# Optimization experiments

Hardware: AMD Instinct MI355X
Metric: run time of the kernel (lower is better)

## Reference

```python
import jax, jax.numpy as jnp
import numpy as np

B, C, N, K = 4, 256, 8192, 16
H, S = 8, 2            # num_heads, num_scale
HC = C // H            # head_channels = 32
CS = C // S            # per-scale channels = 128
HS = H // S            # heads per scale = 4
KV_CH = (64, 128)
EPS = 1e-5
SCALE = HC ** -0.5


def setup_inputs() -> dict:
    key = jax.random.key(0)
    ks = jax.random.split(key, 20)
    d = {}
    d["x"] = jax.random.normal(ks[0], (B, C, N), jnp.float32)
    d["y0"] = jax.random.normal(ks[1], (B, KV_CH[0], N, K), jnp.float32)
    d["y1"] = jax.random.normal(ks[2], (B, KV_CH[1], N, K), jnp.float32)
    d["q_w"] = jax.random.normal(ks[3], (C, C), jnp.float32) * 0.02
    for i, c in enumerate(KV_CH):
        kk = jax.random.split(ks[4 + i], 4)
        d[f"conv{i}_w"] = jax.random.normal(kk[0], (CS, c), jnp.float32) * 0.05  # 1x1 conv
        d[f"bn{i}_g"] = jnp.ones((CS,), jnp.float32)
        d[f"bn{i}_b"] = jnp.zeros((CS,), jnp.float32)
        d[f"bn{i}_m"] = jax.random.normal(kk[1], (CS,), jnp.float32) * 0.1
        d[f"bn{i}_v"] = jax.random.uniform(kk[2], (CS,), jnp.float32) + 0.5
        d[f"kv{i}_w"] = jax.random.normal(kk[3], (2 * CS, CS), jnp.float32) * 0.02
    d["proj_w"] = jax.random.normal(ks[8], (C, C), jnp.float32) * 0.02
    d["proj_b"] = jnp.zeros((C,), jnp.float32)
    return d


def _scale_branch(q_i, y, conv_w, g, b, m, v, kv_w):
    # q_i: [B, HS, N, HC];  y: [B, c, N, K]
    z = jnp.einsum('bcnk,oc->bonk', y, conv_w)                 # 1x1 conv -> [B, CS, N, K]
    inv = (g / jnp.sqrt(v + EPS))[None, :, None, None]
    z = jax.nn.relu((z - m[None, :, None, None]) * inv + b[None, :, None, None])
    kv = jnp.transpose(z, (0, 2, 3, 1)) @ kv_w.T               # [B, N, K, 2*CS]
    kv = kv.reshape(B, N, K, HS, HC, 2)
    k = jnp.transpose(kv[..., 0], (0, 3, 1, 2, 4))             # [B, HS, N, K, HC]
    vv = jnp.transpose(kv[..., 1], (0, 3, 1, 2, 4))            # [B, HS, N, K, HC]
    attn = jax.nn.softmax(jnp.einsum('bhnd,bhnkd->bhnk', q_i, k) * SCALE, axis=-1)
    out = jnp.einsum('bhnk,bhnkd->bhnd', attn, vv)             # [B, HS, N, HC]
    return jnp.transpose(out, (0, 2, 1, 3)).reshape(B, N, HS * HC)


def reference(x, y0, y1, q_w,
              conv0_w, bn0_g, bn0_b, bn0_m, bn0_v, kv0_w,
              conv1_w, bn1_g, bn1_b, bn1_m, bn1_v, kv1_w,
              proj_w, proj_b):
    xt = jnp.swapaxes(x, 1, 2)                                 # [B, N, C]
    q = (xt @ q_w.T).reshape(B, N, H, HC).transpose(0, 2, 1, 3)  # [B, H, N, HC]
    o0 = _scale_branch(q[:, :HS], y0, conv0_w, bn0_g, bn0_b, bn0_m, bn0_v, kv0_w)
    o1 = _scale_branch(q[:, HS:], y1, conv1_w, bn1_g, bn1_b, bn1_m, bn1_v, kv1_w)
    outs = jnp.concatenate([o0, o1], axis=-1)                  # [B, N, C]
    outs = outs @ proj_w.T + proj_b
    return jnp.swapaxes(outs, 1, 2)                            # [B, C, N]
```

## Files before the change

### kernel.cpp

```cpp
#include <hip/hip_runtime.h>
#include <hip/hip_bf16.h>

typedef __attribute__((ext_vector_type(8))) short bf16x8;
typedef __attribute__((ext_vector_type(4))) short bf16x4;
typedef __attribute__((ext_vector_type(4))) float f32x4;
typedef unsigned short ushort_t;
typedef unsigned int uint_t;

__device__ __forceinline__ f32x4 mfma32(bf16x8 a, bf16x8 b, f32x4 c) {
    return __builtin_amdgcn_mfma_f32_16x16x32_bf16(a, b, c, 0, 0, 0);
}
#if __has_builtin(__builtin_amdgcn_mfma_f32_16x16x16bf16_1k)
#define HAVE_MFMA16 1
__device__ __forceinline__ f32x4 mfma16(bf16x4 a, bf16x4 b, f32x4 c) {
    return __builtin_amdgcn_mfma_f32_16x16x16bf16_1k(a, b, c, 0, 0, 0);
}
#else
#define HAVE_MFMA16 0
#endif

namespace {
constexpr int Bn = 4;
constexpr int Nn = 8192;
constexpr float SCALEf = 0.17677669529663687f;
constexpr float EPSf = 1e-5f;

constexpr size_t WS_QW  = 0;
constexpr size_t WS_PW  = 131072;
constexpr size_t WS_KW0 = 262144;
constexpr size_t WS_KW1 = 327680;
constexpr size_t WS_CW0 = 393216;
constexpr size_t WS_CW1 = 409600;
constexpr size_t WS_CB0 = 442368;
constexpr size_t WS_CB1 = 442880;
constexpr size_t WS_AO  = 458752;
}

__device__ __forceinline__ uint_t f2b(float f) {
    union { float f; uint_t u; } v; v.f = f;
    return (v.u + 0x7fffu + ((v.u >> 16) & 1u)) >> 16;
}
__device__ __forceinline__ float b2f(ushort_t u) {
    union { uint_t u; float f; } v; v.u = ((uint_t)u) << 16;
    return v.f;
}
__device__ __forceinline__ uint_t pk2(float lo, float hi) {
    __hip_bfloat162 h = __float22bfloat162_rn(float2{lo, hi});
    union { __hip_bfloat162 h; uint_t u; } v; v.h = h;
    return v.u;
}

template<int KC>
__device__ __forceinline__ int swz(int r, int c) {
    constexpr int SW = (KC / 8 < 16 ? KC / 8 : 16);
    return r * KC + ((((c >> 3) ^ (r & (SW - 1))) << 3) | (c & 7));
}

__global__ void plsa_prep(const float* __restrict__ qw,
                          const float* __restrict__ c0w, const float* __restrict__ g0,
                          const float* __restrict__ b0,  const float* __restrict__ m0,
                          const float* __restrict__ v0,  const float* __restrict__ k0w,
                          const float* __restrict__ c1w, const float* __restrict__ g1,
                          const float* __restrict__ b1,  const float* __restrict__ m1,
                          const float* __restrict__ v1,  const float* __restrict__ k1w,
                          const float* __restrict__ pw,  char* ws) {
    const int i = blockIdx.x * 256 + threadIdx.x;
    ((ushort_t*)(ws + WS_QW))[i] = (ushort_t)f2b(qw[i]);
    ((ushort_t*)(ws + WS_PW))[i] = (ushort_t)f2b(pw[i]);
    if (i < 32768) {
        ((ushort_t*)(ws + WS_KW0))[i] = (ushort_t)f2b(k0w[i]);
        ((ushort_t*)(ws + WS_KW1))[i] = (ushort_t)f2b(k1w[i]);
    }
    if (i < 8192)  { int o = i >> 6;  float inv = g0[o] * rsqrtf(v0[o] + EPSf);
                     ((ushort_t*)(ws + WS_CW0))[i] = (ushort_t)f2b(c0w[i] * inv); }
    if (i < 16384) { int o = i >> 7;  float inv = g1[o] * rsqrtf(v1[o] + EPSf);
                     ((ushort_t*)(ws + WS_CW1))[i] = (ushort_t)f2b(c1w[i] * inv); }
    if (i < 128) {
        float i0 = g0[i] * rsqrtf(v0[i] + EPSf);
        float i1 = g1[i] * rsqrtf(v1[i] + EPSf);
        ((float*)(ws + WS_CB0))[i] = b0[i] - m0[i] * i0;
        ((float*)(ws + WS_CB1))[i] = b1[i] - m1[i] * i1;
    }
}

template<int CIN>
__device__ __forceinline__ void issue_y2(const float* __restrict__ yb, int b, int n0c,
                                         float* yreg, int tid) {
    constexpr int ITER = CIN / 16;
    #pragma unroll
    for (int it = 0; it < ITER; ++it) {
        const int idx = tid + it * 256;
        const int pk = idx & 31, c0 = (idx >> 5) * 2;
        const float* ysrc = yb + ((size_t)(b * CIN + c0)) * (Nn * 16)
                               + (size_t)(n0c + (pk >> 4)) * 16 + (pk & 15);
        yreg[it * 2]     = ysrc[0];
        yreg[it * 2 + 1] = ysrc[(size_t)Nn * 16];
    }
}
template<int CIN>
__device__ __forceinline__ void write_y2(ushort_t* Ys, const float* yreg, int tid) {
    constexpr int ITER = CIN / 16;
    #pragma unroll
    for (int it = 0; it < ITER; ++it) {
        const int idx = tid + it * 256;
        const int pk = idx & 31, c0 = (idx >> 5) * 2;
        *(uint_t*)(Ys + swz<CIN>(pk, c0)) = pk2(yreg[it * 2], yreg[it * 2 + 1]);
    }
}

template<int CIN, int NCIN>
__device__ __forceinline__ void branch_run(
    int tid, int b, int n0,
    const float* __restrict__ yb, const float* __restrict__ ynext,
    const char* __restrict__ ws,
    ushort_t* Ys, ushort_t* Zs, ushort_t* Ks, ushort_t* Vs,
    const ushort_t* qs, ushort_t* aobuf, float* yreg)
{
    constexpr size_t wcw = (CIN == 64) ? WS_CW0 : WS_CW1;
    constexpr size_t wcb = (CIN == 64) ? WS_CB0 : WS_CB1;
    constexpr size_t wkw = (CIN == 64) ? WS_KW0 : WS_KW1;
    constexpr int qb = (CIN == 64) ? 0 : 128;
    constexpr int KT = CIN / 32;

    const ushort_t* cwb = (const ushort_t*)(ws + wcw);
    const float*    cbb = (const float*)(ws + wcb);
    const ushort_t* kwb = (const ushort_t*)(ws + wkw);
    const int w = tid >> 6, lane = tid & 63, l15 = lane & 15, lk = lane >> 4;

    #pragma unroll 1
    for (int cc = 0; cc < 8; ++cc) {
        if (cc < 7) issue_y2<CIN>(yb, b, n0 + (cc + 1) * 2, yreg, tid);
        else if constexpr (NCIN != 0) issue_y2<NCIN>(ynext, b, n0, yreg, tid);

        #pragma unroll
        for (int ct = 0; ct < 2; ++ct) {
            bf16x8 bfr[KT];
            #pragma unroll
            for (int k = 0; k < KT; ++k)
                bfr[k] = *(const bf16x8*)(Ys + swz<CIN>(ct * 16 + l15, k * 32 + lk * 8));
            #pragma unroll
            for (int mi = 0; mi < 2; ++mi) {
                f32x4 a = f32x4{0.f, 0.f, 0.f, 0.f};
                #pragma unroll
                for (int k = 0; k < KT; ++k) {
                    bf16x8 af = *(const bf16x8*)(cwb + ((w * 2 + mi) * 16 + l15) * CIN + k * 32 + lk * 8);
                    a = mfma32(af, bfr[k], a);
                }
                const int col = ct * 16 + l15, o0 = (w * 2 + mi) * 16 + lk * 4;
                const float4 cb4 = *(const float4*)(cbb + (w * 2 + mi) * 16 + lk * 4);
                const float z0 = fmaxf(a.x + cb4.x, 0.f);
                const float z1 = fmaxf(a.y + cb4.y, 0.f);
                const float z2 = fmaxf(a.z + cb4.z, 0.f);
                const float z3 = fmaxf(a.w + cb4.w, 0.f);
                const int off = swz<128>(col, o0);
                *(uint_t*)(Zs + off)     = pk2(z0, z1);
                *(uint_t*)(Zs + off + 2) = pk2(z2, z3);
            }
        }
        __syncthreads();

        #pragma unroll
        for (int ct = 0; ct < 2; ++ct) {
            bf16x8 bfr[4];
            #pragma unroll
            for (int k = 0; k < 4; ++k)
                bfr[k] = *(const bf16x8*)(Zs + swz<128>(ct * 16 + l15, k * 32 + lk * 8));
            const int col = ct * 16 + l15;
            #pragma unroll
            for (int mi = 0; mi < 4; ++mi) {
                f32x4 a = f32x4{0.f, 0.f, 0.f, 0.f};
                #pragma unroll
                for (int k = 0; k < 4; ++k) {
                    bf16x8 af = *(const bf16x8*)(kwb + ((w * 4 + mi) * 16 + l15) * 128 + k * 32 + lk * 8);
                    a = mfma32(af, bfr[k], a);
                }
                const int j0 = (w * 4 + mi) * 16 + lk * 4;
                const int h = j0 >> 6;
                const int d0 = (j0 & 63) >> 1;
                *(uint_t*)(Ks + swz<128>(col, h * 32 + d0)) = pk2(a.x, a.z);
                const uint_t vv = pk2(a.y, a.w);
                Vs[swz<32>(h * 32 + d0,     col)] = (ushort_t)vv;
                Vs[swz<32>(h * 32 + d0 + 1, col)] = (ushort_t)(vv >> 16);
            }
        }
        if (cc < 7) write_y2<CIN>(Ys, yreg, tid);
        else if constexpr (NCIN != 0) write_y2<NCIN>(Ys, yreg, tid);
        __syncthreads();

#if HAVE_MFMA16
        {
            const int pt = w >> 1, pr = w & 1;
            #pragma unroll
            for (int hh = 0; hh < 2; ++hh) {
                const int h = pr * 2 + hh;
                bf16x8 ka  = *(const bf16x8*)(Ks + swz<128>(pt * 16 + l15, h * 32 + lk * 8));
                bf16x8 qf  = *(const bf16x8*)(qs + swz<256>(cc * 2 + pt, qb + h * 32 + lk * 8));
                f32x4 zero = f32x4{0.f, 0.f, 0.f, 0.f};
                f32x4 sc = mfma32(ka, qf, zero);
                float s0 = sc.x * SCALEf, s1 = sc.y * SCALEf;
                float s2 = sc.z * SCALEf, s3 = sc.w * SCALEf;
                float mx = fmaxf(fmaxf(s0, s1), fmaxf(s2, s3));
                mx = fmaxf(mx, __shfl_xor(mx, 16));
                mx = fmaxf(mx, __shfl_xor(mx, 32));
                float e0 = __expf(s0 - mx), e1 = __expf(s1 - mx);
                float e2 = __expf(s2 - mx), e3 = __expf(s3 - mx);
                float t = e0 + e1 + e2 + e3;
                t += __shfl_xor(t, 16);
                t += __shfl_xor(t, 32);
                const float r = 1.f / t;
                union { uint_t u[2]; bf16x4 v; } pf;
                pf.u[0] = pk2(e0 * r, e1 * r);
                pf.u[1] = pk2(e2 * r, e3 * r);
                #pragma unroll
                for (int dblk = 0; dblk < 2; ++dblk) {
                    bf16x4 va = *(const bf16x4*)(Vs + swz<32>(h * 32 + dblk * 16 + l15, pt * 16 + lk * 4));
                    f32x4 o = mfma16(va, pf.v, zero);
                    if (l15 == 0) {
                        uint2 ou;
                        ou.x = pk2(o.x, o.y);
                        ou.y = pk2(o.z, o.w);
                        *(uint2*)(aobuf + ((size_t)(b * Nn + n0 + cc * 2 + pt)) * 256
                                  + qb + h * 32 + dblk * 16 + lk * 4) = ou;
                    }
                }
            }
        }
#else
        {
            const int pt = w >> 1, pr = w & 1;
            float p = 0.f;
            if (lane < 32) {
                const int kk = lane & 15;
                const int h = pr * 2 + (lane >> 4);
                float s = 0.f;
                #pragma unroll
                for (int dc = 0; dc < 4; ++dc) {
                    bf16x8 q8 = *(const bf16x8*)(qs + swz<256>(cc * 2 + pt, qb + h * 32 + dc * 8));
                    bf16x8 k8 = *(const bf16x8*)(Ks + swz<128>(pt * 16 + kk, h * 32 + dc * 8));
                    #pragma unroll
                    for (int j = 0; j < 8; ++j)
                        s += b2f((ushort_t)q8[j]) * b2f((ushort_t)k8[j]);
                }
                s *= SCALEf;
                float mx = s;
                #pragma unroll
                for (int m = 1; m < 16; m <<= 1) mx = fmaxf(mx, __shfl_xor(mx, m));
                const float e = __expf(s - mx);
                float sum = e;
                #pragma unroll
                for (int m = 1; m < 16; m <<= 1) sum += __shfl_xor(sum, m);
                p = e / sum;
            }
            const int d = lane & 31, hh2 = lane >> 5;
            const int h2 = pr * 2 + hh2;
            const int row = h2 * 32 + d;
            bf16x8 va = *(const bf16x8*)(Vs + swz<32>(row, pt * 16));
            bf16x8 vb = *(const bf16x8*)(Vs + swz<32>(row, pt * 16 + 8));
            float o = 0.f;
            #pragma unroll
            for (int j = 0; j < 8; ++j) {
                o += __shfl(p, hh2 * 16 + j)     * b2f((ushort_t)va[j]);
                o += __shfl(p, hh2 * 16 + 8 + j) * b2f((ushort_t)vb[j]);
            }
            aobuf[((size_t)(b * Nn + n0 + cc * 2 + pt)) * 256 + qb + h2 * 32 + d] = (ushort_t)f2b(o);
        }
#endif
    }
}

__global__ __launch_bounds__(256, 2) void k_attn(
    const float* __restrict__ x, const float* __restrict__ y0, const float* __restrict__ y1,
    const char* __restrict__ ws, ushort_t* __restrict__ aobuf) {

    __shared__ __align__(16) ushort_t qs[4096];
    __shared__ __align__(16) ushort_t Ys[4096];
    __shared__ __align__(16) ushort_t Zs[4096];
    __shared__ __align__(16) ushort_t Ks[4096];
    __shared__ __align__(16) ushort_t Vs[4096];

    const int tid = threadIdx.x;
    const int b = blockIdx.x >> 9, n0 = (blockIdx.x & 511) << 4;
    const int w = tid >> 6, lane = tid & 63, l15 = lane & 15, lk = lane >> 4;
    float yreg[16];

    const int xn = tid & 15, cg = tid >> 4;
    #pragma unroll
    for (int hseg = 0; hseg < 2; ++hseg) {
        float xreg[8];
        #pragma unroll
        for (int i = 0; i < 8; ++i)
            xreg[i] = x[((size_t)(b * 256 + cg * 16 + hseg * 8 + i)) * Nn + n0 + xn];
        #pragma unroll
        for (int j = 0; j < 4; ++j)
            *(uint_t*)(Ys + swz<256>(xn, cg * 16 + hseg * 8 + 2 * j)) =
                pk2(xreg[2 * j], xreg[2 * j + 1]);
    }
    issue_y2<64>(y0, b, n0, yreg, tid);
    __syncthreads();

    {
        const ushort_t* qwb = (const ushort_t*)(ws + WS_QW);
        #pragma unroll
        for (int mi = 0; mi < 4; ++mi) {
            f32x4 acc = f32x4{0.f, 0.f, 0.f, 0.f};
            #pragma unroll
            for (int k = 0; k < 8; ++k) {
                bf16x8 af = *(const bf16x8*)(qwb + ((w * 4 + mi) * 16 + l15) * 256 + k * 32 + lk * 8);
                bf16x8 bf = *(const bf16x8*)(Ys + swz<256>(l15, k * 32 + lk * 8));
                acc = mfma32(af, bf, acc);
            }
            const int ch0 = (w * 4 + mi) * 16 + lk * 4;
            uint2 u;
            u.x = pk2(acc.x, acc.y);
            u.y = pk2(acc.z, acc.w);
            *(uint2*)(qs + swz<256>(l15, ch0)) = u;
        }
    }
    __syncthreads();

    write_y2<64>(Ys, yreg, tid);
    __syncthreads();

    branch_run<64, 128>(tid, b, n0, y0, y1, ws, Ys, Zs, Ks, Vs, qs, aobuf, yreg);
    branch_run<128, 0> (tid, b, n0, y1, nullptr, ws, Ys, Zs, Ks, Vs, qs, aobuf, yreg);
}

__global__ __launch_bounds__(256, 2) void k_proj(const char* __restrict__ ws,
                                                 const float* __restrict__ proj_b,
                                                 float* __restrict__ out) {
    __shared__ __align__(16) ushort_t At[64 * 256];
    const ushort_t* pwb = (const ushort_t*)(ws + WS_PW);
    const ushort_t* aobuf = (const ushort_t*)(ws + WS_AO);
    const int tid = threadIdx.x;
    const int b = blockIdx.x >> 7, n0 = (blockIdx.x & 127) * 64;

    {
        const int cp = tid & 127, ng = tid >> 7;
        #pragma unroll
        for (int i = 0; i < 32; ++i) {
            const int n = ng + i * 2;
            const uint_t u = *(const uint_t*)(aobuf + ((size_t)(b * Nn + n0 + n)) * 256 + cp * 2);
            *(uint_t*)(At + swz<256>(n, cp * 2)) = u;
        }
    }
    __syncthreads();

    const int w = tid >> 6, lane = tid & 63, l15 = lane & 15, lk = lane >> 4;
    #pragma unroll
    for (int mi = 0; mi < 4; ++mi) {
        bf16x8 af[8];
        #pragma unroll
        for (int k = 0; k < 8; ++k)
            af[k] = *(const bf16x8*)(pwb + (w * 64 + mi * 16 + l15) * 256 + k * 32 + lk * 8);
        const int ch0 = w * 64 + mi * 16 + lk * 4;
        const float4 pbv = *(const float4*)(proj_b + ch0);
        #pragma unroll
        for (int ct = 0; ct < 4; ++ct) {
            f32x4 acc = f32x4{0.f, 0.f, 0.f, 0.f};
            #pragma unroll
            for (int k = 0; k < 8; ++k) {
                bf16x8 bf = *(const bf16x8*)(At + swz<256>(ct * 16 + l15, k * 32 + lk * 8));
                acc = mfma32(af[k], bf, acc);
            }
            const int nn = n0 + ct * 16 + l15;
            out[((size_t)(b * 256 + ch0 + 0)) * Nn + nn] = acc.x + pbv.x;
            out[((size_t)(b * 256 + ch0 + 1)) * Nn + nn] = acc.y + pbv.y;
            out[((size_t)(b * 256 + ch0 + 2)) * Nn + nn] = acc.z + pbv.z;
            out[((size_t)(b * 256 + ch0 + 3)) * Nn + nn] = acc.w + pbv.w;
        }
    }
}

extern "C" void kernel_launch(void* const* d_in, const int* in_sizes, int n_in,
                              void* d_out, int out_size, void* d_ws, size_t ws_size,
                              hipStream_t stream) {
    const float* x       = (const float*)d_in[0];
    const float* y0      = (const float*)d_in[1];
    const float* y1      = (const float*)d_in[2];
    const float* q_w     = (const float*)d_in[3];
    const float* conv0_w = (const float*)d_in[4];
    const float* bn0_g   = (const float*)d_in[5];
    const float* bn0_b   = (const float*)d_in[6];
    const float* bn0_m   = (const float*)d_in[7];
    const float* bn0_v   = (const float*)d_in[8];
    const float* kv0_w   = (const float*)d_in[9];
    const float* conv1_w = (const float*)d_in[10];
    const float* bn1_g   = (const float*)d_in[11];
    const float* bn1_b   = (const float*)d_in[12];
    const float* bn1_m   = (const float*)d_in[13];
    const float* bn1_v   = (const float*)d_in[14];
    const float* kv1_w   = (const float*)d_in[15];
    const float* proj_w  = (const float*)d_in[16];
    const float* proj_b  = (const float*)d_in[17];
    char* ws = (char*)d_ws;

    plsa_prep<<<256, 256, 0, stream>>>(q_w, conv0_w, bn0_g, bn0_b, bn0_m, bn0_v, kv0_w,
                                       conv1_w, bn1_g, bn1_b, bn1_m, bn1_v, kv1_w,
                                       proj_w, ws);
    k_attn<<<Bn * (Nn / 16), 256, 0, stream>>>(x, y0, y1, ws,
                                               (ushort_t*)(ws + WS_AO));
    k_proj<<<Bn * (Nn / 64), 256, 0, stream>>>(ws, proj_b, (float*)d_out);
}
```

Measured before the change: 253.7 us.

## Process four points per pipeline stage instead of two in attention kernel

Each inner-loop iteration of the branch pipeline now handles 4 query points (64 key columns) instead of 2, halving the number of iterations and the barriers between them. The shared buffers for Y, Z, K and V are doubled, and each wave now owns one point across all four heads in the attention step. This should amortise barriers and weight-fragment loads over more columns, at the cost of roughly double the LDS use and register pressure (yreg grows to 32 floats), which may lower occupancy below the two blocks per CU the launch bounds ask for.

```diff
diff --git a/kernel.cpp b/kernel.cpp
--- a/kernel.cpp
+++ b/kernel.cpp
@@ -84,13 +84,13 @@
 }
 
 template<int CIN>
-__device__ __forceinline__ void issue_y2(const float* __restrict__ yb, int b, int n0c,
+__device__ __forceinline__ void issue_y4(const float* __restrict__ yb, int b, int n0c,
                                          float* yreg, int tid) {
-    constexpr int ITER = CIN / 16;
+    constexpr int ITER = CIN / 8;
     #pragma unroll
     for (int it = 0; it < ITER; ++it) {
         const int idx = tid + it * 256;
-        const int pk = idx & 31, c0 = (idx >> 5) * 2;
+        const int pk = idx & 63, c0 = (idx >> 6) * 2;
         const float* ysrc = yb + ((size_t)(b * CIN + c0)) * (Nn * 16)
                                + (size_t)(n0c + (pk >> 4)) * 16 + (pk & 15);
         yreg[it * 2]     = ysrc[0];
@@ -98,12 +98,12 @@
     }
 }
 template<int CIN>
-__device__ __forceinline__ void write_y2(ushort_t* Ys, const float* yreg, int tid) {
-    constexpr int ITER = CIN / 16;
+__device__ __forceinline__ void write_y4(ushort_t* Ys, const float* yreg, int tid) {
+    constexpr int ITER = CIN / 8;
     #pragma unroll
     for (int it = 0; it < ITER; ++it) {
         const int idx = tid + it * 256;
-        const int pk = idx & 31, c0 = (idx >> 5) * 2;
+        const int pk = idx & 63, c0 = (idx >> 6) * 2;
         *(uint_t*)(Ys + swz<CIN>(pk, c0)) = pk2(yreg[it * 2], yreg[it * 2 + 1]);
     }
 }
@@ -128,12 +128,12 @@
     const int w = tid >> 6, lane = tid & 63, l15 = lane & 15, lk = lane >> 4;
 
     #pragma unroll 1
-    for (int cc = 0; cc < 8; ++cc) {
-        if (cc < 7) issue_y2<CIN>(yb, b, n0 + (cc + 1) * 2, yreg, tid);
-        else if constexpr (NCIN != 0) issue_y2<NCIN>(ynext, b, n0, yreg, tid);
-
-        #pragma unroll
-        for (int ct = 0; ct < 2; ++ct) {
+    for (int cc = 0; cc < 4; ++cc) {
+        if (cc < 3) issue_y4<CIN>(yb, b, n0 + (cc + 1) * 4, yreg, tid);
+        else if constexpr (NCIN != 0) issue_y4<NCIN>(ynext, b, n0, yreg, tid);
+
+        #pragma unroll
+        for (int ct = 0; ct < 4; ++ct) {
             bf16x8 bfr[KT];
             #pragma unroll
             for (int k = 0; k < KT; ++k)
@@ -160,7 +160,7 @@
         __syncthreads();
 
         #pragma unroll
-        for (int ct = 0; ct < 2; ++ct) {
+        for (int ct = 0; ct < 4; ++ct) {
             bf16x8 bfr[4];
             #pragma unroll
             for (int k = 0; k < 4; ++k)
@@ -179,22 +179,21 @@
                 const int d0 = (j0 & 63) >> 1;
                 *(uint_t*)(Ks + swz<128>(col, h * 32 + d0)) = pk2(a.x, a.z);
                 const uint_t vv = pk2(a.y, a.w);
-                Vs[swz<32>(h * 32 + d0,     col)] = (ushort_t)vv;
-                Vs[swz<32>(h * 32 + d0 + 1, col)] = (ushort_t)(vv >> 16);
-            }
-        }
-        if (cc < 7) write_y2<CIN>(Ys, yreg, tid);
-        else if constexpr (NCIN != 0) write_y2<NCIN>(Ys, yreg, tid);
+                Vs[swz<64>(h * 32 + d0,     col)] = (ushort_t)vv;
+                Vs[swz<64>(h * 32 + d0 + 1, col)] = (ushort_t)(vv >> 16);
+            }
+        }
+        if (cc < 3) write_y4<CIN>(Ys, yreg, tid);
+        else if constexpr (NCIN != 0) write_y4<NCIN>(Ys, yreg, tid);
         __syncthreads();
 
 #if HAVE_MFMA16
         {
-            const int pt = w >> 1, pr = w & 1;
-            #pragma unroll
-            for (int hh = 0; hh < 2; ++hh) {
-                const int h = pr * 2 + hh;
+            const int pt = w;
+            #pragma unroll
+            for (int h = 0; h < 4; ++h) {
                 bf16x8 ka  = *(const bf16x8*)(Ks + swz<128>(pt * 16 + l15, h * 32 + lk * 8));
-                bf16x8 qf  = *(const bf16x8*)(qs + swz<256>(cc * 2 + pt, qb + h * 32 + lk * 8));
+                bf16x8 qf  = *(const bf16x8*)(qs + swz<256>(cc * 4 + pt, qb + h * 32 + lk * 8));
                 f32x4 zero = f32x4{0.f, 0.f, 0.f, 0.f};
                 f32x4 sc = mfma32(ka, qf, zero);
                 float s0 = sc.x * SCALEf, s1 = sc.y * SCALEf;
@@ -213,13 +212,13 @@
                 pf.u[1] = pk2(e2 * r, e3 * r);
                 #pragma unroll
                 for (int dblk = 0; dblk < 2; ++dblk) {
-                    bf16x4 va = *(const bf16x4*)(Vs + swz<32>(h * 32 + dblk * 16 + l15, pt * 16 + lk * 4));
+                    bf16x4 va = *(const bf16x4*)(Vs + swz<64>(h * 32 + dblk * 16 + l15, pt * 16 + lk * 4));
                     f32x4 o = mfma16(va, pf.v, zero);
                     if (l15 == 0) {
                         uint2 ou;
                         ou.x = pk2(o.x, o.y);
                         ou.y = pk2(o.z, o.w);
-                        *(uint2*)(aobuf + ((size_t)(b * Nn + n0 + cc * 2 + pt)) * 256
+                        *(uint2*)(aobuf + ((size_t)(b * Nn + n0 + cc * 4 + pt)) * 256
                                   + qb + h * 32 + dblk * 16 + lk * 4) = ou;
                     }
                 }
@@ -227,42 +226,45 @@
         }
 #else
         {
-            const int pt = w >> 1, pr = w & 1;
-            float p = 0.f;
-            if (lane < 32) {
-                const int kk = lane & 15;
-                const int h = pr * 2 + (lane >> 4);
-                float s = 0.f;
+            const int pt = w;
+            #pragma unroll
+            for (int hp = 0; hp < 2; ++hp) {
+                float p = 0.f;
+                if (lane < 32) {
+                    const int kk = lane & 15;
+                    const int h = hp * 2 + (lane >> 4);
+                    float s = 0.f;
+                    #pragma unroll
+                    for (int dc = 0; dc < 4; ++dc) {
+                        bf16x8 q8 = *(const bf16x8*)(qs + swz<256>(cc * 4 + pt, qb + h * 32 + dc * 8));
+                        bf16x8 k8 = *(const bf16x8*)(Ks + swz<128>(pt * 16 + kk, h * 32 + dc * 8));
+                        #pragma unroll
+                        for (int j = 0; j < 8; ++j)
+                            s += b2f((ushort_t)q8[j]) * b2f((ushort_t)k8[j]);
+                    }
+                    s *= SCALEf;
+                    float mx = s;
+                    #pragma unroll
+                    for (int m = 1; m < 16; m <<= 1) mx = fmaxf(mx, __shfl_xor(mx, m));
+                    const float e = __expf(s - mx);
+                    float sum = e;
+                    #pragma unroll
+                    for (int m = 1; m < 16; m <<= 1) sum += __shfl_xor(sum, m);
+                    p = e / sum;
+                }
+                const int d = lane & 31, hh2 = lane >> 5;
+                const int h2 = hp * 2 + hh2;
+                const int row = h2 * 32 + d;
+                bf16x8 va = *(const bf16x8*)(Vs + swz<64>(row, pt * 16));
+                bf16x8 vb = *(const bf16x8*)(Vs + swz<64>(row, pt * 16 + 8));
+                float o = 0.f;
                 #pragma unroll
-                for (int dc = 0; dc < 4; ++dc) {
-                    bf16x8 q8 = *(const bf16x8*)(qs + swz<256>(cc * 2 + pt, qb + h * 32 + dc * 8));
-                    bf16x8 k8 = *(const bf16x8*)(Ks + swz<128>(pt * 16 + kk, h * 32 + dc * 8));
-                    #pragma unroll
-                    for (int j = 0; j < 8; ++j)
-                        s += b2f((ushort_t)q8[j]) * b2f((ushort_t)k8[j]);
+                for (int j = 0; j < 8; ++j) {
+                    o += __shfl(p, hh2 * 16 + j)     * b2f((ushort_t)va[j]);
+                    o += __shfl(p, hh2 * 16 + 8 + j) * b2f((ushort_t)vb[j]);
                 }
-                s *= SCALEf;
-                float mx = s;
-                #pragma unroll
-                for (int m = 1; m < 16; m <<= 1) mx = fmaxf(mx, __shfl_xor(mx, m));
-                const float e = __expf(s - mx);
-                float sum = e;
-                #pragma unroll
-                for (int m = 1; m < 16; m <<= 1) sum += __shfl_xor(sum, m);
-                p = e / sum;
-            }
-            const int d = lane & 31, hh2 = lane >> 5;
-            const int h2 = pr * 2 + hh2;
-            const int row = h2 * 32 + d;
-            bf16x8 va = *(const bf16x8*)(Vs + swz<32>(row, pt * 16));
-            bf16x8 vb = *(const bf16x8*)(Vs + swz<32>(row, pt * 16 + 8));
-            float o = 0.f;
-            #pragma unroll
-            for (int j = 0; j < 8; ++j) {
-                o += __shfl(p, hh2 * 16 + j)     * b2f((ushort_t)va[j]);
-                o += __shfl(p, hh2 * 16 + 8 + j) * b2f((ushort_t)vb[j]);
-            }
-            aobuf[((size_t)(b * Nn + n0 + cc * 2 + pt)) * 256 + qb + h2 * 32 + d] = (ushort_t)f2b(o);
+                aobuf[((size_t)(b * Nn + n0 + cc * 4 + pt)) * 256 + qb + h2 * 32 + d] = (ushort_t)f2b(o);
+            }
         }
 #endif
     }
@@ -273,15 +275,15 @@
     const char* __restrict__ ws, ushort_t* __restrict__ aobuf) {
 
     __shared__ __align__(16) ushort_t qs[4096];
-    __shared__ __align__(16) ushort_t Ys[4096];
-    __shared__ __align__(16) ushort_t Zs[4096];
-    __shared__ __align__(16) ushort_t Ks[4096];
-    __shared__ __align__(16) ushort_t Vs[4096];
+    __shared__ __align__(16) ushort_t Ys[8192];
+    __shared__ __align__(16) ushort_t Zs[8192];
+    __shared__ __align__(16) ushort_t Ks[8192];
+    __shared__ __align__(16) ushort_t Vs[8192];
 
     const int tid = threadIdx.x;
     const int b = blockIdx.x >> 9, n0 = (blockIdx.x & 511) << 4;
     const int w = tid >> 6, lane = tid & 63, l15 = lane & 15, lk = lane >> 4;
-    float yreg[16];
+    float yreg[32];
 
     const int xn = tid & 15, cg = tid >> 4;
     #pragma unroll
@@ -295,7 +297,7 @@
             *(uint_t*)(Ys + swz<256>(xn, cg * 16 + hseg * 8 + 2 * j)) =
                 pk2(xreg[2 * j], xreg[2 * j + 1]);
     }
-    issue_y2<64>(y0, b, n0, yreg, tid);
+    issue_y4<64>(y0, b, n0, yreg, tid);
     __syncthreads();
 
     {
@@ -318,7 +320,7 @@
     }
     __syncthreads();
 
-    write_y2<64>(Ys, yreg, tid);
+    write_y4<64>(Ys, yreg, tid);
     __syncthreads();
 
     branch_run<64, 128>(tid, b, n0, y0, y1, ws, Ys, Zs, Ks, Vs, qs, aobuf, yreg);
```

New measurement: 505.9 us. 1.99x slower.

## Halve y prefetch registers, raise occupancy, and use LDS-only barriers

Applied to the files above, without the earlier changes.

The register buffer for prefetched y tiles is halved. For the 128-channel branch the prefetch is split into two halves: the first is written to shared memory right after the conv stage barrier, and the second is issued then and written after the KV stage. This cuts register pressure so launch bounds can go from 2 to 3 blocks per CU. Full __syncthreads are replaced by a barrier that waits only on LDS and scalar counters, so global loads stay in flight across it. The cost is shorter prefetch lead time for the second half and possible spills at the tighter register budget.

```diff
diff --git a/kernel.cpp b/kernel.cpp
--- a/kernel.cpp
+++ b/kernel.cpp
@@ -18,6 +18,11 @@
 #else
 #define HAVE_MFMA16 0
 #endif
+
+__device__ __forceinline__ void softbar() {
+    asm volatile("s_waitcnt lgkmcnt(0)" ::: "memory");
+    __builtin_amdgcn_s_barrier();
+}
 
 namespace {
 constexpr int Bn = 4;
@@ -83,28 +88,26 @@
     }
 }
 
-template<int CIN>
-__device__ __forceinline__ void issue_y2(const float* __restrict__ yb, int b, int n0c,
-                                         float* yreg, int tid) {
-    constexpr int ITER = CIN / 16;
+template<int CIN, int IT0, int IT1>
+__device__ __forceinline__ void issue_y2_r(const float* __restrict__ yb, int b, int n0c,
+                                           float* yreg, int tid) {
     #pragma unroll
-    for (int it = 0; it < ITER; ++it) {
+    for (int it = IT0; it < IT1; ++it) {
         const int idx = tid + it * 256;
         const int pk = idx & 31, c0 = (idx >> 5) * 2;
         const float* ysrc = yb + ((size_t)(b * CIN + c0)) * (Nn * 16)
                                + (size_t)(n0c + (pk >> 4)) * 16 + (pk & 15);
-        yreg[it * 2]     = ysrc[0];
-        yreg[it * 2 + 1] = ysrc[(size_t)Nn * 16];
-    }
-}
-template<int CIN>
-__device__ __forceinline__ void write_y2(ushort_t* Ys, const float* yreg, int tid) {
-    constexpr int ITER = CIN / 16;
+        yreg[(it - IT0) * 2]     = ysrc[0];
+        yreg[(it - IT0) * 2 + 1] = ysrc[(size_t)Nn * 16];
+    }
+}
+template<int CIN, int IT0, int IT1>
+__device__ __forceinline__ void write_y2_r(ushort_t* Ys, const float* yreg, int tid) {
     #pragma unroll
-    for (int it = 0; it < ITER; ++it) {
+    for (int it = IT0; it < IT1; ++it) {
         const int idx = tid + it * 256;
         const int pk = idx & 31, c0 = (idx >> 5) * 2;
-        *(uint_t*)(Ys + swz<CIN>(pk, c0)) = pk2(yreg[it * 2], yreg[it * 2 + 1]);
+        *(uint_t*)(Ys + swz<CIN>(pk, c0)) = pk2(yreg[(it - IT0) * 2], yreg[(it - IT0) * 2 + 1]);
     }
 }
 
@@ -129,8 +132,8 @@
 
     #pragma unroll 1
     for (int cc = 0; cc < 8; ++cc) {
-        if (cc < 7) issue_y2<CIN>(yb, b, n0 + (cc + 1) * 2, yreg, tid);
-        else if constexpr (NCIN != 0) issue_y2<NCIN>(ynext, b, n0, yreg, tid);
+        if (cc < 7) issue_y2_r<CIN, 0, (CIN == 64 ? 4 : 4)>(yb, b, n0 + (cc + 1) * 2, yreg, tid);
+        else if constexpr (NCIN != 0) issue_y2_r<NCIN, 0, 4>(ynext, b, n0, yreg, tid);
 
         #pragma unroll
         for (int ct = 0; ct < 2; ++ct) {
@@ -157,7 +160,15 @@
                 *(uint_t*)(Zs + off + 2) = pk2(z2, z3);
             }
         }
-        __syncthreads();
+        softbar();
+
+        if (cc < 7) {
+            write_y2_r<CIN, 0, 4>(Ys, yreg, tid);
+            if constexpr (CIN == 128) issue_y2_r<CIN, 4, 8>(yb, b, n0 + (cc + 1) * 2, yreg, tid);
+        } else if constexpr (NCIN != 0) {
+            write_y2_r<NCIN, 0, 4>(Ys, yreg, tid);
+            if constexpr (NCIN == 128) issue_y2_r<NCIN, 4, 8>(ynext, b, n0, yreg, tid);
+        }
 
         #pragma unroll
         for (int ct = 0; ct < 2; ++ct) {
@@ -183,9 +194,9 @@
                 Vs[swz<32>(h * 32 + d0 + 1, col)] = (ushort_t)(vv >> 16);
             }
         }
-        if (cc < 7) write_y2<CIN>(Ys, yreg, tid);
-        else if constexpr (NCIN != 0) write_y2<NCIN>(Ys, yreg, tid);
-        __syncthreads();
+        if (cc < 7) { if constexpr (CIN == 128) write_y2_r<CIN, 4, 8>(Ys, yreg, tid); }
+        else if constexpr (NCIN == 128) write_y2_r<NCIN, 4, 8>(Ys, yreg, tid);
+        softbar();
 
 #if HAVE_MFMA16
         {
@@ -268,7 +279,7 @@
     }
 }
 
-__global__ __launch_bounds__(256, 2) void k_attn(
+__global__ __launch_bounds__(256, 3) void k_attn(
     const float* __restrict__ x, const float* __restrict__ y0, const float* __restrict__ y1,
     const char* __restrict__ ws, ushort_t* __restrict__ aobuf) {
 
@@ -281,21 +292,21 @@
     const int tid = threadIdx.x;
     const int b = blockIdx.x >> 9, n0 = (blockIdx.x & 511) << 4;
     const int w = tid >> 6, lane = tid & 63, l15 = lane & 15, lk = lane >> 4;
-    float yreg[16];
+    float yreg[8];
 
     const int xn = tid & 15, cg = tid >> 4;
     #pragma unroll
-    for (int hseg = 0; hseg < 2; ++hseg) {
-        float xreg[8];
-        #pragma unroll
-        for (int i = 0; i < 8; ++i)
-            xreg[i] = x[((size_t)(b * 256 + cg * 16 + hseg * 8 + i)) * Nn + n0 + xn];
-        #pragma unroll
-        for (int j = 0; j < 4; ++j)
-            *(uint_t*)(Ys + swz<256>(xn, cg * 16 + hseg * 8 + 2 * j)) =
+    for (int qseg = 0; qseg < 4; ++qseg) {
+        float xreg[4];
+        #pragma unroll
+        for (int i = 0; i < 4; ++i)
+            xreg[i] = x[((size_t)(b * 256 + cg * 16 + qseg * 4 + i)) * Nn + n0 + xn];
+        #pragma unroll
+        for (int j = 0; j < 2; ++j)
+            *(uint_t*)(Ys + swz<256>(xn, cg * 16 + qseg * 4 + 2 * j)) =
                 pk2(xreg[2 * j], xreg[2 * j + 1]);
     }
-    issue_y2<64>(y0, b, n0, yreg, tid);
+    issue_y2_r<64, 0, 4>(y0, b, n0, yreg, tid);
     __syncthreads();
 
     {
@@ -318,7 +329,7 @@
     }
     __syncthreads();
 
-    write_y2<64>(Ys, yreg, tid);
+    write_y2_r<64, 0, 4>(Ys, yreg, tid);
     __syncthreads();
 
     branch_run<64, 128>(tid, b, n0, y0, y1, ws, Ys, Zs, Ks, Vs, qs, aobuf, yreg);
```

New measurement: 822.9 us. 224% more time.
